# Kernel optimization log

Measured on AMD Instinct MI355X. Metric: run time of the kernel, lower is better.

Reference implementation:

```python
import jax, jax.numpy as jnp
import numpy as np

B, S, D_TEXT, MAXF = 2, 1024, 384, 5
D_MODEL, N_HEADS, D_FF, L = 768, 12, 3072, 4
HEAD_DIM = D_MODEL // N_HEADS
EPS = 1e-6
NEG = -1e9


def _rms(x, g):
    return x * jax.lax.rsqrt(jnp.mean(x * x, axis=-1, keepdims=True) + EPS) * g


def _attn(x, w, mask):
    # w: [4, d, d] = (wq, wk, wv, wo); mask: [b, s, s] bool (True = attend)
    b, s, d = x.shape

    def proj(W):
        return jnp.einsum('bsd,de->bse', x, W).reshape(b, s, N_HEADS, HEAD_DIM).transpose(0, 2, 1, 3)

    q, k, v = proj(w[0]), proj(w[1]), proj(w[2])
    scale = jnp.asarray(1.0 / np.sqrt(HEAD_DIM), x.dtype)
    scores = jnp.einsum('bhqe,bhke->bhqk', q, k) * scale
    scores = jnp.where(mask[:, None], scores, NEG)
    p = jax.nn.softmax(scores, axis=-1)
    o = jnp.einsum('bhqk,bhke->bhqe', p, v).transpose(0, 2, 1, 3).reshape(b, s, d)
    return jnp.einsum('bsd,de->bse', o, w[3])


def _forward(number_values, datetime_values, boolean_values, text_values, column_name_values,
             W_cn, b_cn, W_num, b_num, W_text, b_text, W_dt, b_dt, W_bool, b_bool,
             g_cn, g_num, g_text, g_dt, g_bool, mask_emb,
             blk_norms, blk_attn, blk_up, blk_gate, blk_down,
             g_out, Wd_num, bd_num, Wd_dt, bd_dt, Wd_bool, bd_bool, Wd_text, bd_text,
             node_indices, table_name_indices, column_name_indices,
             f2p_neighbor_indices, semantic_types, masks, is_padding):
    valid = ~is_padding
    pv = valid[:, :, None] & valid[:, None, :]  # [b,s,s]
    eye = jnp.eye(S, dtype=bool)[None]
    same_node = node_indices[:, :, None] == node_indices[:, None, :]
    col_mask = ((column_name_indices[:, :, None] == column_name_indices[:, None, :])
                & (table_name_indices[:, :, None] == table_name_indices[:, None, :]) & pv) | eye
    feat_mask = (same_node & pv) | eye
    # kv node is one of q's f2p neighbors
    nei = (f2p_neighbor_indices[:, :, :, None] == node_indices[:, None, None, :]).any(axis=2)
    nei_mask = ((nei | same_node) & pv) | eye
    full_mask = pv | eye

    # per-semantic-type value encoders (Linear + RMSNorm)
    cn = _rms(column_name_values @ W_cn + b_cn, g_cn)
    num_e = _rms(number_values @ W_num + b_num, g_num)
    text_e = _rms(text_values @ W_text + b_text, g_text)
    dt_e = _rms(datetime_values @ W_dt + b_dt, g_dt)
    bool_e = _rms(boolean_values @ W_bool + b_bool, g_bool)
    st = semantic_types[..., None]
    val = jnp.where(st == 0, num_e, jnp.where(st == 1, text_e, jnp.where(st == 2, dt_e, bool_e)))
    # masked cells get the learned mask embedding for their semantic type
    val = jnp.where(masks[..., None], mask_emb[semantic_types], val)
    x = val + cn

    for i in range(L):
        nw, aw = blk_norms[i], blk_attn[i]
        x = x + _attn(_rms(x, nw[0]), aw[0], col_mask)
        x = x + _attn(_rms(x, nw[1]), aw[1], feat_mask)
        x = x + _attn(_rms(x, nw[2]), aw[2], nei_mask)
        x = x + _attn(_rms(x, nw[3]), aw[3], full_mask)
        h = _rms(x, nw[4])
        x = x + (jax.nn.silu(h @ blk_gate[i]) * (h @ blk_up[i])) @ blk_down[i]

    h = _rms(x, g_out)
    return (h @ Wd_num + bd_num, h @ Wd_dt + bd_dt, h @ Wd_bool + bd_bool, h @ Wd_text + bd_text)


def setup_inputs() -> dict:
    key = jax.random.key(0)
    ks = iter(jax.random.split(key, 64))

    def nrm(shape, scale=0.02):
        return jax.random.normal(next(ks), shape, jnp.float32) * scale

    inp = {}
    inp['number_values'] = jax.random.normal(next(ks), (B, S, 1), jnp.float32)
    inp['datetime_values'] = jax.random.normal(next(ks), (B, S, 1), jnp.float32)
    inp['boolean_values'] = jax.random.normal(next(ks), (B, S, 1), jnp.float32)
    inp['text_values'] = jax.random.normal(next(ks), (B, S, D_TEXT), jnp.float32)
    inp['column_name_values'] = jax.random.normal(next(ks), (B, S, D_TEXT), jnp.float32)
    inp['W_cn'] = nrm((D_TEXT, D_MODEL)); inp['b_cn'] = jnp.zeros((D_MODEL,), jnp.float32)
    inp['W_num'] = nrm((1, D_MODEL)); inp['b_num'] = jnp.zeros((D_MODEL,), jnp.float32)
    inp['W_text'] = nrm((D_TEXT, D_MODEL)); inp['b_text'] = jnp.zeros((D_MODEL,), jnp.float32)
    inp['W_dt'] = nrm((1, D_MODEL)); inp['b_dt'] = jnp.zeros((D_MODEL,), jnp.float32)
    inp['W_bool'] = nrm((1, D_MODEL)); inp['b_bool'] = jnp.zeros((D_MODEL,), jnp.float32)
    for n in ('g_cn', 'g_num', 'g_text', 'g_dt', 'g_bool'):
        inp[n] = jnp.ones((D_MODEL,), jnp.float32)
    inp['mask_emb'] = jax.random.normal(next(ks), (4, D_MODEL), jnp.float32)
    inp['blk_norms'] = jnp.ones((L, 5, D_MODEL), jnp.float32)
    inp['blk_attn'] = nrm((L, 4, 4, D_MODEL, D_MODEL))
    inp['blk_up'] = nrm((L, D_MODEL, D_FF))
    inp['blk_gate'] = nrm((L, D_MODEL, D_FF))
    inp['blk_down'] = nrm((L, D_FF, D_MODEL))
    inp['g_out'] = jnp.ones((D_MODEL,), jnp.float32)
    inp['Wd_num'] = nrm((D_MODEL, 1)); inp['bd_num'] = jnp.zeros((1,), jnp.float32)
    inp['Wd_dt'] = nrm((D_MODEL, 1)); inp['bd_dt'] = jnp.zeros((1,), jnp.float32)
    inp['Wd_bool'] = nrm((D_MODEL, 1)); inp['bd_bool'] = jnp.zeros((1,), jnp.float32)
    inp['Wd_text'] = nrm((D_MODEL, D_TEXT)); inp['bd_text'] = jnp.zeros((D_TEXT,), jnp.float32)
    inp['node_indices'] = jax.random.randint(next(ks), (B, S), 0, 128)
    inp['table_name_indices'] = jax.random.randint(next(ks), (B, S), 0, 8)
    inp['column_name_indices'] = jax.random.randint(next(ks), (B, S), 0, 32)
    inp['f2p_neighbor_indices'] = jax.random.randint(next(ks), (B, S, MAXF), 0, 128)
    inp['semantic_types'] = jax.random.randint(next(ks), (B, S), 0, 4)
    inp['masks'] = jax.random.bernoulli(next(ks), 0.15, (B, S))
    inp['is_padding'] = jnp.zeros((B, S), bool)
    return inp


def reference(number_values, datetime_values, boolean_values, text_values, column_name_values,
              W_cn, b_cn, W_num, b_num, W_text, b_text, W_dt, b_dt, W_bool, b_bool,
              g_cn, g_num, g_text, g_dt, g_bool, mask_emb,
              blk_norms, blk_attn, blk_up, blk_gate, blk_down,
              g_out, Wd_num, bd_num, Wd_dt, bd_dt, Wd_bool, bd_bool, Wd_text, bd_text,
              node_indices, table_name_indices, column_name_indices,
              f2p_neighbor_indices, semantic_types, masks, is_padding):
    return _forward(number_values, datetime_values, boolean_values, text_values, column_name_values,
                    W_cn, b_cn, W_num, b_num, W_text, b_text, W_dt, b_dt, W_bool, b_bool,
                    g_cn, g_num, g_text, g_dt, g_bool, mask_emb,
                    blk_norms, blk_attn, blk_up, blk_gate, blk_down,
                    g_out, Wd_num, bd_num, Wd_dt, bd_dt, Wd_bool, bd_bool, Wd_text, bd_text,
                    node_indices, table_name_indices, column_name_indices,
                    f2p_neighbor_indices, semantic_types, masks, is_padding)
```

## Files before the change

### kernel.cpp

```cpp
#include <hip/hip_runtime.h>
#include <hip/hip_bf16.h>
#include <cmath>
#include <stdint.h>


#define BB 2
#define SS 1024
#define DT 384
#define DM 768
#define NH 12
#define DH 64
#define DFF 3072
#define NL 4
#define NROW (BB*SS)
#define EPSF 1e-6f
#define NEGF (-1e9f)

typedef unsigned short u16;
typedef unsigned char u8;
typedef unsigned int u32;
typedef __attribute__((ext_vector_type(8))) short s16x8;
typedef __attribute__((ext_vector_type(4))) float f32x4;

__device__ __forceinline__ u16 f2bu(float f){
    u32 x = __float_as_uint(f);
    u32 r = (x + 0x7fffu + ((x>>16)&1u)) >> 16;
    return (u16)r;
}
__device__ __forceinline__ u32 pk2(float lo, float hi){
    return (u32)f2bu(lo) | ((u32)f2bu(hi)<<16);
}
__device__ __forceinline__ int swz(int row, int c){
    return (row<<6) + (((((c>>3) ^ row) & 7))<<3) + (c&7);
}
__device__ __forceinline__ float rsum16(float v){
    v += __shfl_xor(v,1); v += __shfl_xor(v,2);
    v += __shfl_xor(v,4); v += __shfl_xor(v,8);
    return v;
}
#define SBAR() __builtin_amdgcn_sched_barrier(0)
#define GLDS(src,dst) __builtin_amdgcn_global_load_lds((const __attribute__((address_space(1))) u32*)(src), (__attribute__((address_space(3))) u32*)(dst), 16, 0, 0)
#define GLDS4(src,dst) __builtin_amdgcn_global_load_lds((const __attribute__((address_space(1))) u32*)(src), (__attribute__((address_space(3))) u32*)(dst), 4, 0, 0)

__global__ void zero_f(float* __restrict__ p, int n){
    int i = blockIdx.x*256 + threadIdx.x;
    if (i<n) p[i]=0.f;
}

__global__ void norm_bool_kernel(const void* __restrict__ src, u8* __restrict__ dst, int n)
{
    __shared__ int fl[4];
    if (threadIdx.x<4) fl[threadIdx.x]=0;
    __syncthreads();
    const u32* wsrc = (const u32*)src;
    const int nw = n/4;
    int any=0, nb=0, hi=0, lo=0;
    for (int i=threadIdx.x;i<nw;i+=blockDim.x){
        u32 v=wsrc[i];
        if (!v) continue;
        any=1;
        #pragma unroll
        for (int b=0;b<4;b++){
            u32 by=(v>>(8*b))&0xffu;
            if (by>1u) nb=1;
            if (by==1u && b!=0) hi=1;
        }
        if ((v&0xffffu)==0x3f80u) lo=1;
    }
    if (any) atomicOr(&fl[0],1);
    if (nb)  atomicOr(&fl[1],1);
    if (hi)  atomicOr(&fl[2],1);
    if (lo)  atomicOr(&fl[3],1);
    __syncthreads();
    int c;
    if (!fl[0]) c=0;
    else if (!fl[1]) c = fl[2] ? 2 : 1;
    else if (fl[3]) c = 3;
    else c = 1;
    for (int i=threadIdx.x;i<n;i+=blockDim.x){
        u8 v;
        if (c==0)      v=0;
        else if (c==1) v = (((const u32*)src)[i]!=0u);
        else if (c==2) v = (((const u8*)src)[i]!=0u);
        else           v = (((const u16*)src)[i]!=0u);
        dst[i]=v;
    }
}

__global__ void pack_meta(const int* __restrict__ node, const int* __restrict__ colx,
                          const int* __restrict__ tbl, const u8* __restrict__ pad,
                          u32* __restrict__ pm, int n)
{
    int i = blockIdx.x*256 + threadIdx.x;
    if (i<n)
        pm[i] = (u32)(node[i]&0xff) | ((u32)(colx[i]&0xff)<<8) | ((u32)(tbl[i]&0xff)<<16) | ((u32)(pad[i]&1)<<24);
}

__global__ __launch_bounds__(256) void mask4_kernel(const u32* __restrict__ pm, const int* __restrict__ f2p,
                                                    u8* __restrict__ m4)
{
    const int b = blockIdx.y, kg = blockIdx.x;
    const int t = threadIdx.x;
    __shared__ u32 qm[1024];
    __shared__ int qf[1024*5];
    for (int i=t;i<1024;i+=256) qm[i] = pm[b*SS+i];
    for (int i=t;i<5*1024;i+=256) qf[i] = f2p[b*SS*5 + i];
    __syncthreads();
    const int q0 = t*4;
    u32 qmv[4]; int qn[4]; int qfv[4][5];
    #pragma unroll
    for (int j=0;j<4;j++){
        qmv[j]=qm[q0+j]; qn[j]=(int)(qmv[j]&0xffu);
        #pragma unroll
        for (int f=0;f<5;f++) qfv[j][f]=qf[(q0+j)*5+f];
    }
    for (int kk=0;kk<16;kk++){
        const int k = kg*16+kk;
        const u32 km = qm[k];
        const int kn = (int)(km&0xffu);
        u32 outw=0;
        #pragma unroll
        for (int j=0;j<4;j++){
            const u32 qmw = qmv[j];
            const bool pv = (((qmw|km)>>24)&1u)==0u;
            u32 by=0;
            if ((((qmw^km)&0x00ffff00u)==0u) && pv) by|=1;
            if ((((qmw^km)&0xffu)==0u) && pv) by|=2;
            bool nei = (qfv[j][0]==kn)||(qfv[j][1]==kn)||(qfv[j][2]==kn)||(qfv[j][3]==kn)||(qfv[j][4]==kn)
                       ||(qn[j]==kn);
            if (nei && pv) by|=4;
            if (pv) by|=8;
            if ((q0+j)==k) by=15;
            outw |= by<<(8*j);
        }
        ((u32*)(m4 + ((size_t)b<<20) + ((size_t)k<<10)))[t] = outw;
    }
}

__global__ __launch_bounds__(256) void transpose_cvt2(const float* __restrict__ src, u16* __restrict__ dst,
                                                      int K, int N, size_t dz,
                                                      const float* __restrict__ gbase, int gmode)
{
    const int z = blockIdx.z;
    src += (size_t)z*K*N;
    dst += (size_t)z*dz;
    const float* g = nullptr;
    if (gmode==1){ int m = z&3; if (m<3) g = gbase + (size_t)((z>>4)*5 + ((z>>2)&3))*768; }
    else if (gmode==2){ g = gbase + (size_t)z*5*768; }
    const int n0 = blockIdx.x*32, k0 = blockIdx.y*64;
    __shared__ float t[64][33];
    const int tid = threadIdx.x;
    const int kr = tid>>3, n4 = (tid&7)*4;
    #pragma unroll
    for (int p=0;p<2;p++){
        const int k = p*32 + kr;
        float gk = g ? g[k0+k] : 1.f;
        float4 v = *(const float4*)(src + (size_t)(k0+k)*N + n0 + n4);
        t[k][n4]=v.x*gk; t[k][n4+1]=v.y*gk; t[k][n4+2]=v.z*gk; t[k][n4+3]=v.w*gk;
    }
    __syncthreads();
    const int n = tid>>3, ks = (tid&7)*8;
    const int ng = n0 + n;
    uint4 o;
    u32* op = (u32*)&o;
    #pragma unroll
    for (int i=0;i<4;i++)
        op[i] = pk2(t[ks+2*i][n], t[ks+2*i+1][n]);
    *(uint4*)&dst[(((size_t)(ng>>7)*(K>>6) + (k0>>6))<<13) + ((ng&127)<<6) + ks] = o;
}

__global__ __launch_bounds__(256) void cvt_tiled(const float* __restrict__ src, u16* __restrict__ dst, int K)
{
    const int gid = blockIdx.x*256 + threadIdx.x;
    const int base = gid*8;
    const int row = base / K, col = base - row*K;
    float4 a = *(const float4*)(src + base);
    float4 b = *(const float4*)(src + base + 4);
    uint4 o;
    o.x = pk2(a.x,a.y); o.y = pk2(a.z,a.w);
    o.z = pk2(b.x,b.y); o.w = pk2(b.z,b.w);
    *(uint4*)&dst[(((size_t)(row>>7)*(K>>6) + (col>>6))<<13) + ((row&127)<<6) + (col&63)] = o;
}

__device__ __forceinline__ void stage3(const u16* aT, const u16* bT, int cb, int brow,
                                       u16* la, u16* lb, int w, int l)
{
    #pragma unroll
    for (int p=0;p<2;p++){
        const int q = p*256 + w*64 + l;
        const int row = q>>2, u = q&3;
        const int so = row*64 + cb + (((u ^ ((row>>1)&3))&3)<<3);
        GLDS(aT+so, la + p*2048 + w*512);
    }
    {
        const int q = w*64 + l;
        const int row = q>>2, u = q&3;
        const int so = (brow+row)*64 + cb + (((u ^ ((row>>1)&3))&3)<<3);
        GLDS(bT+so, lb + w*512);
    }
}

__global__ __launch_bounds__(256,4) void gemm_t(
    const u16* __restrict__ At, const u16* __restrict__ Bt, float* __restrict__ C,
    int N, int K, int AMS, int flags, const float* __restrict__ bias,
    u16* __restrict__ o16, u16* __restrict__ qk16, u16* __restrict__ vt16,
    const float* __restrict__ rs_in, float* __restrict__ rs_out)
{
    __shared__ u16 lds[3][6144];
    const int tid = threadIdx.x;
    const int lane = tid & 63, w = tid >> 6;
    const int cg = lane >> 4, cl = lane & 15;
    const int NT = K >> 5;
    const int n0 = blockIdx.x*64;
    const int brow = n0 & 64;
    const size_t bNb = (size_t)(n0>>7)*(K>>6);

    const u16* aB = At + ((size_t)blockIdx.y * AMS << 13);
    const u16* bB = Bt + (bNb << 13);

    f32x4 acc[2][4];
    #pragma unroll
    for (int i=0;i<2;i++)
        #pragma unroll
        for (int j=0;j<4;j++) acc[i][j] = (f32x4){0.f,0.f,0.f,0.f};

    stage3(aB, bB, 0,  brow, &lds[0][0], &lds[0][4096], w, lane);
    stage3(aB, bB, 32, brow, &lds[1][0], &lds[1][4096], w, lane);

    for (int kt=0; kt<NT; kt++){
        const int buf = kt % 3;
        if (kt+2 < NT){
            const int k2 = kt+2;
            stage3(aB + ((size_t)(k2>>1)<<13), bB + ((size_t)(k2>>1)<<13),
                   (k2&1)<<5, brow, &lds[k2%3][0], &lds[k2%3][4096], w, lane);
            asm volatile("s_waitcnt vmcnt(6)" ::: "memory");
        } else if (kt+1 < NT){
            asm volatile("s_waitcnt vmcnt(3)" ::: "memory");
        } else {
            asm volatile("s_waitcnt vmcnt(0)" ::: "memory");
        }
        SBAR(); __builtin_amdgcn_s_barrier(); SBAR();
        s16x8 af[2], bf[4];
        #pragma unroll
        for (int mt=0;mt<2;mt++){
            const int ra = w*32 + mt*16 + cl;
            af[mt] = *(const s16x8*)&lds[buf][ra*32 + (((cg ^ ((ra>>1)&3))&3)<<3)];
        }
        #pragma unroll
        for (int nt=0;nt<4;nt++){
            const int rb = nt*16 + cl;
            bf[nt] = *(const s16x8*)&lds[buf][4096 + rb*32 + (((cg ^ ((rb>>1)&3))&3)<<3)];
        }
        #pragma unroll
        for (int mt=0;mt<2;mt++)
            #pragma unroll
            for (int nt=0;nt<4;nt++)
                acc[mt][nt] = __builtin_amdgcn_mfma_f32_16x16x32_bf16(af[mt], bf[nt], acc[mt][nt], 0,0,0);
        SBAR(); __builtin_amdgcn_s_barrier(); SBAR();
    }

    const int m0 = blockIdx.y*128;
    if (flags & 4){
        #pragma unroll
        for (int mt=0;mt<2;mt++){
            const int grow0 = m0 + w*32 + mt*16 + cg*4;
            float rr[4];
            #pragma unroll
            for (int j=0;j<4;j++) rr[j] = rsqrtf(rs_in[grow0+j]*(1.f/768.f) + EPSF);
            #pragma unroll
            for (int nt=0;nt<4;nt++){
                const int col = n0 + nt*16 + cl;
                if (col < 1536){
                    #pragma unroll
                    for (int j=0;j<4;j++)
                        qk16[(size_t)(grow0+j)*1536 + col] = f2bu(acc[mt][nt][j]*rr[j]);
                } else {
                    const int b = grow0>>10, s0 = grow0&1023;
                    const int dhg = col - 1536;
                    uint2 o;
                    o.x = pk2(acc[mt][nt][0]*rr[0], acc[mt][nt][1]*rr[1]);
                    o.y = pk2(acc[mt][nt][2]*rr[2], acc[mt][nt][3]*rr[3]);
                    *(uint2*)(vt16 + ((size_t)(b*768 + dhg)<<10) + s0) = o;
                }
            }
        }
    } else {
        const int NC = N>>6;
        #pragma unroll
        for (int mt=0;mt<2;mt++){
            const int grow0 = m0 + w*32 + mt*16 + cg*4;
            float rr[4];
            #pragma unroll
            for (int j=0;j<4;j++) rr[j] = rs_in ? rsqrtf(rs_in[grow0+j]*(1.f/768.f) + EPSF) : 1.f;
            #pragma unroll
            for (int nt=0;nt<4;nt++){
                const int col = n0 + nt*16 + cl;
                const size_t tb = (((size_t)(grow0>>7)*NC + (col>>6))<<13) + (col&63);
                #pragma unroll
                for (int j=0;j<4;j++)
                    o16[tb + (((grow0+j)&127)<<6)] = f2bu(acc[mt][nt][j]*rr[j]);
            }
        }
    }
}

__device__ __forceinline__ void stage64(const u16* aT, int arow, const u16* bT, int brow, int cb,
                                        u16* la, u16* lb, int w, int l)
{
    const int q = w*64 + l;
    const int row = q>>2, u = q&3;
    const int sw = (((u ^ ((row>>1)&3))&3)<<3);
    GLDS(aT + (arow+row)*64 + cb + sw, la + w*512);
    GLDS(bT + (brow+row)*64 + cb + sw, lb + w*512);
}

__global__ __launch_bounds__(256,6) void gemm_t64(
    const u16* __restrict__ At, const u16* __restrict__ Bt, float* __restrict__ C,
    int N, int K, int AMS, int flags, const float* __restrict__ bias,
    u16* __restrict__ o16, float* __restrict__ rs_out)
{
    __shared__ u16 lds[3][4096];
    const int tid = threadIdx.x;
    const int lane = tid & 63, w = tid >> 6;
    const int cg = lane >> 4, cl = lane & 15;
    const int NT = K >> 5;
    const int n0 = blockIdx.x*64;
    const int m0 = blockIdx.y*64;
    const int brow = n0 & 64, arow = m0 & 64;

    const u16* aB = At + ((size_t)(m0>>7) * AMS << 13);
    const u16* bB = Bt + ((size_t)(n0>>7) * (K>>6) << 13);

    f32x4 acc[4];
    #pragma unroll
    for (int j=0;j<4;j++) acc[j] = (f32x4){0.f,0.f,0.f,0.f};

    stage64(aB, arow, bB, brow, 0,  &lds[0][0], &lds[0][2048], w, lane);
    stage64(aB, arow, bB, brow, 32, &lds[1][0], &lds[1][2048], w, lane);

    for (int kt=0; kt<NT; kt++){
        const int buf = kt % 3;
        if (kt+2 < NT){
            const int k2 = kt+2;
            stage64(aB + ((size_t)(k2>>1)<<13), arow, bB + ((size_t)(k2>>1)<<13), brow,
                    (k2&1)<<5, &lds[k2%3][0], &lds[k2%3][2048], w, lane);
            asm volatile("s_waitcnt vmcnt(4)" ::: "memory");
        } else if (kt+1 < NT){
            asm volatile("s_waitcnt vmcnt(2)" ::: "memory");
        } else {
            asm volatile("s_waitcnt vmcnt(0)" ::: "memory");
        }
        SBAR(); __builtin_amdgcn_s_barrier(); SBAR();
        const int ra = w*16 + cl;
        s16x8 af = *(const s16x8*)&lds[buf][ra*32 + (((cg ^ ((ra>>1)&3))&3)<<3)];
        s16x8 bf[4];
        #pragma unroll
        for (int nt=0;nt<4;nt++){
            const int rb = nt*16 + cl;
            bf[nt] = *(const s16x8*)&lds[buf][2048 + rb*32 + (((cg ^ ((rb>>1)&3))&3)<<3)];
        }
        #pragma unroll
        for (int nt=0;nt<4;nt++)
            acc[nt] = __builtin_amdgcn_mfma_f32_16x16x32_bf16(af, bf[nt], acc[nt], 0,0,0);
        SBAR(); __builtin_amdgcn_s_barrier(); SBAR();
    }

    const int grow0 = m0 + w*16 + cg*4;
    const bool do_acc = (flags&1), do_bias = (flags&2);
    float tmp[4][4];
    #pragma unroll
    for (int nt=0;nt<4;nt++){
        const int col = n0 + nt*16 + cl;
        float bv = do_bias ? bias[col] : 0.f;
        #pragma unroll
        for (int j=0;j<4;j++){
            float v = acc[nt][j] + bv;
            float* cp = C + (size_t)(grow0+j)*N + col;
            if (do_acc) v += *cp;
            *cp = v;
            tmp[nt][j] = v;
        }
    }
    if (o16){
        #pragma unroll
        for (int nt=0;nt<4;nt++){
            const int col = n0 + nt*16 + cl;
            const size_t tb = (((size_t)(grow0>>7)*12 + (col>>6))<<13) + (col&63);
            #pragma unroll
            for (int j=0;j<4;j++)
                o16[tb + (((grow0+j)&127)<<6)] = f2bu(tmp[nt][j]);
        }
    }
    if (rs_out){
        #pragma unroll
        for (int j=0;j<4;j++){
            float s = tmp[0][j]*tmp[0][j] + tmp[1][j]*tmp[1][j]
                    + tmp[2][j]*tmp[2][j] + tmp[3][j]*tmp[3][j];
            s = rsum16(s);
            if (cl==0) atomicAdd(rs_out + grow0 + j, s);
        }
    }
}

__global__ __launch_bounds__(256,3) void attn_mfma3(
    const u16* __restrict__ qk16, const u16* __restrict__ vt16,
    const u8* __restrict__ m4, int mt,
    u16* __restrict__ ob16)
{
    const int bh = blockIdx.y;
    const int b = bh / NH, h = bh % NH;
    const int q0 = blockIdx.x * 64;
    const int tid = threadIdx.x;
    const int w = tid>>6, lane = tid&63, cg = lane>>4, cl = lane&15;
    const int srow = lane>>3;
    const int sseg = (lane&7) ^ srow;
    const int mk = lane>>4, mq = lane&15;

    __shared__ u16 Qs[4096], Ks[2][4096], Vt[2][4096], Ps[4096];
    __shared__ u32 Ms[2][1024];

    const u16* qbase = qk16 + (size_t)(b*SS+q0)*1536 + h*64;
    const u16* kbase = qk16 + (size_t)(b*SS)*1536 + 768 + h*64;
    const u16* vbase = vt16 + ((size_t)(b*768 + h*64)<<10);
    const u8*  mbase = m4 + ((size_t)b<<20) + q0;

    #pragma unroll
    for (int p=0;p<2;p++){
        const int row = p*32 + w*8 + srow;
        GLDS(qbase + (size_t)row*1536 + sseg*8, Qs + p*2048 + w*512);
    }
    #pragma unroll
    for (int p=0;p<2;p++){
        const int row = p*32 + w*8 + srow;
        GLDS(kbase + (size_t)row*1536 + sseg*8, Ks[0] + p*2048 + w*512);
        GLDS(vbase + ((size_t)row<<10) + sseg*8, Vt[0] + p*2048 + w*512);
    }
    #pragma unroll
    for (int i=0;i<4;i++){
        const int key = w*16 + i*4 + mk;
        GLDS4(mbase + ((size_t)key<<10) + mq*4, (u8*)Ms[0] + w*1024 + i*256);
    }

    f32x4 o[4];
    #pragma unroll
    for (int nt=0;nt<4;nt++) o[nt] = (f32x4){0.f,0.f,0.f,0.f};
    float lsum[4] = {0.f,0.f,0.f,0.f};

    for (int kc=0;kc<16;kc++){
        const int buf = kc & 1;
        if (kc < 15){
            const int kn0 = kc*64 + 64;
            #pragma unroll
            for (int p=0;p<2;p++){
                const int row = p*32 + w*8 + srow;
                GLDS(kbase + (size_t)(kn0+row)*1536 + sseg*8, Ks[buf^1] + p*2048 + w*512);
                GLDS(vbase + ((size_t)row<<10) + kn0 + sseg*8, Vt[buf^1] + p*2048 + w*512);
            }
            #pragma unroll
            for (int i=0;i<4;i++){
                const int key = kn0 + w*16 + i*4 + mk;
                GLDS4(mbase + ((size_t)key<<10) + mq*4, (u8*)Ms[buf^1] + w*1024 + i*256);
            }
            asm volatile("s_waitcnt vmcnt(8)" ::: "memory");
        } else {
            asm volatile("s_waitcnt vmcnt(0)" ::: "memory");
        }
        SBAR(); __builtin_amdgcn_s_barrier(); SBAR();

        f32x4 sc[4];
        #pragma unroll
        for (int nt=0;nt<4;nt++) sc[nt] = (f32x4){0.f,0.f,0.f,0.f};
        __builtin_amdgcn_s_setprio(1);
        #pragma unroll
        for (int ks=0;ks<2;ks++){
            s16x8 qa = *(const s16x8*)&Qs[swz(w*16+cl, ks*32+cg*8)];
            #pragma unroll
            for (int nt=0;nt<4;nt++){
                s16x8 kb = *(const s16x8*)&Ks[buf][swz(nt*16+cl, ks*32+cg*8)];
                sc[nt] = __builtin_amdgcn_mfma_f32_16x16x32_bf16(qa, kb, sc[nt], 0,0,0);
            }
        }
        __builtin_amdgcn_s_setprio(0);

        float pP[4][4];
        #pragma unroll
        for (int nt=0;nt<4;nt++){
            const u32 w4 = Ms[buf][(nt*16+cl)*16 + w*4 + cg];
            #pragma unroll
            for (int j=0;j<4;j++){
                float sv = fminf(sc[nt][j]*0.125f, 60.f);
                float pe = __expf(sv);
                pe = ((w4 >> (8*j + mt)) & 1u) ? pe : 0.f;
                pP[nt][j] = pe;
                lsum[j] += pe;
            }
        }

        #pragma unroll
        for (int nt=0;nt<4;nt++)
            #pragma unroll
            for (int j=0;j<4;j++)
                Ps[swz(w*16+cg*4+j, nt*16+cl)] = f2bu(pP[nt][j]);

        __builtin_amdgcn_s_setprio(1);
        #pragma unroll
        for (int ks=0;ks<2;ks++){
            s16x8 pa = *(const s16x8*)&Ps[swz(w*16+cl, ks*32+cg*8)];
            #pragma unroll
            for (int nt=0;nt<4;nt++){
                s16x8 vb = *(const s16x8*)&Vt[buf][swz(nt*16+cl, ks*32+cg*8)];
                o[nt] = __builtin_amdgcn_mfma_f32_16x16x32_bf16(pa, vb, o[nt], 0,0,0);
            }
        }
        __builtin_amdgcn_s_setprio(0);
        SBAR(); __builtin_amdgcn_s_barrier(); SBAR();
    }

    #pragma unroll
    for (int j=0;j<4;j++){
        const float inv = 1.f/rsum16(lsum[j]);
        const int row = b*SS + q0 + w*16 + cg*4 + j;
        const size_t rb = ((size_t)(row>>7)*12 + h)*8192 + ((row&127)<<6);
        #pragma unroll
        for (int nt=0;nt<4;nt++)
            ob16[rb + nt*16 + cl] = f2bu(o[nt][j]*inv);
    }
}

__global__ __launch_bounds__(256) void fuse_encode(
    const float* __restrict__ cnbuf, const float* __restrict__ textbuf,
    const float* __restrict__ numv, const float* __restrict__ dtv, const float* __restrict__ boolv,
    const float* __restrict__ Wnum, const float* __restrict__ bnum,
    const float* __restrict__ Wdt, const float* __restrict__ bdt,
    const float* __restrict__ Wbool, const float* __restrict__ bbool,
    const float* __restrict__ gcn, const float* __restrict__ gnum, const float* __restrict__ gtext,
    const float* __restrict__ gdt, const float* __restrict__ gbool,
    const float* __restrict__ memb, const int* __restrict__ stypes, const u8* __restrict__ masks,
    float* __restrict__ x, u16* __restrict__ xt16, float* __restrict__ rs0)
{
    const int row = blockIdx.x;
    const int t = threadIdx.x;
    __shared__ float red[256];

    float cn3[3]; float ss=0.f;
    #pragma unroll
    for (int j=0;j<3;j++){
        cn3[j] = cnbuf[(size_t)row*DM + t + j*256];
        ss += cn3[j]*cn3[j];
    }
    red[t]=ss; __syncthreads();
    for (int s=128;s>0;s>>=1){ if(t<s) red[t]+=red[t+s]; __syncthreads(); }
    {
        float r = rsqrtf(red[0]/(float)DM + EPSF);
        #pragma unroll
        for (int j=0;j<3;j++) cn3[j] *= r*gcn[t+j*256];
    }
    __syncthreads();

    const int st = stypes[row];
    float val[3]; ss=0.f;
    if (st==1){
        #pragma unroll
        for (int j=0;j<3;j++){
            val[j] = textbuf[(size_t)row*DM + t + j*256];
            ss += val[j]*val[j];
        }
    } else {
        const float* Wp = (st==0)?Wnum:((st==2)?Wdt:Wbool);
        const float* bp = (st==0)?bnum:((st==2)?bdt:bbool);
        const float* vp = (st==0)?numv:((st==2)?dtv:boolv);
        float v = vp[row];
        #pragma unroll
        for (int j=0;j<3;j++){
            int e=t+j*256;
            val[j] = v*Wp[e] + bp[e];
            ss += val[j]*val[j];
        }
    }
    red[t]=ss; __syncthreads();
    for (int s=128;s>0;s>>=1){ if(t<s) red[t]+=red[t+s]; __syncthreads(); }
    const float* gp = (st==0)?gnum:((st==1)?gtext:((st==2)?gdt:gbool));
    float r2 = rsqrtf(red[0]/(float)DM + EPSF);
    bool mk = masks[row]!=0;
    float xv[3]; float sx=0.f;
    #pragma unroll
    for (int j=0;j<3;j++){
        int e=t+j*256;
        float vv = val[j]*r2*gp[e];
        if (mk) vv = memb[st*DM+e];
        xv[j] = vv + cn3[j];
        x[(size_t)row*DM+e] = xv[j];
        sx += xv[j]*xv[j];
    }
    __syncthreads();
    red[t]=sx; __syncthreads();
    for (int s=128;s>0;s>>=1){ if(t<s) red[t]+=red[t+s]; __syncthreads(); }
    if (t==0) rs0[row] = red[0];
    const size_t mb = (size_t)(row>>7)*12;
    const int rr = (row&127)<<6;
    #pragma unroll
    for (int j=0;j<3;j++){
        const int c = t + j*256;
        xt16[((mb + (c>>6))<<13) + rr + (c&63)] = f2bu(xv[j]);
    }
}

__global__ void silu_gu(u16* __restrict__ gu, int nu)
{
    int i = blockIdx.x*blockDim.x + threadIdx.x;
    const int stride = gridDim.x*blockDim.x;
    for (; i<nu; i+=stride){
        const int mt = i / (48*1024);
        const int r  = i - mt*48*1024;
        const size_t gi = (size_t)(mt*96)*1024 + r;
        const size_t ui = gi + 48*1024;
        uint4 gv = ((const uint4*)gu)[gi];
        uint4 uv = ((const uint4*)gu)[ui];
        u32 go[4]; const u32* gp=(const u32*)&gv; const u32* up=(const u32*)&uv;
        #pragma unroll
        for (int k=0;k<4;k++){
            float g0 = __uint_as_float(gp[k]<<16), g1 = __uint_as_float(gp[k]&0xffff0000u);
            float u0 = __uint_as_float(up[k]<<16), u1 = __uint_as_float(up[k]&0xffff0000u);
            float s0 = g0/(1.f+__expf(-g0))*u0;
            float s1 = g1/(1.f+__expf(-g1))*u1;
            go[k] = pk2(s0, s1);
        }
        ((uint4*)gu)[gi] = make_uint4(go[0],go[1],go[2],go[3]);
    }
}

__global__ __launch_bounds__(256) void decode2(
    const float* __restrict__ x, const float* __restrict__ gout,
    const float* __restrict__ Wn, const float* __restrict__ bn,
    const float* __restrict__ Wd, const float* __restrict__ bd,
    const float* __restrict__ Wb, const float* __restrict__ bb,
    float* __restrict__ out, u16* __restrict__ h16)
{
    const int row = blockIdx.x;
    const int t = threadIdx.x;
    __shared__ float h[DM];
    __shared__ float red[256];
    const float* xr = x + (size_t)row*DM;
    float v0=xr[t], v1=xr[t+256], v2=xr[t+512];
    red[t]=v0*v0+v1*v1+v2*v2; __syncthreads();
    for (int s=128;s>0;s>>=1){ if(t<s) red[t]+=red[t+s]; __syncthreads(); }
    float r = rsqrtf(red[0]/(float)DM + EPSF);
    float h0 = v0*r*gout[t], h1 = v1*r*gout[t+256], h2 = v2*r*gout[t+512];
    h[t]=h0; h[t+256]=h1; h[t+512]=h2;
    const size_t mb = (size_t)(row>>7)*12;
    const int rr = (row&127)<<6;
    #pragma unroll
    for (int j=0;j<3;j++){
        const int c = t + j*256;
        const float v = (j==0?h0:(j==1?h1:h2));
        h16[((mb + (c>>6))<<13) + rr + (c&63)] = f2bu(v);
    }
    __syncthreads();

    float pn=0.f,pd=0.f,pb=0.f;
    for (int k=t;k<DM;k+=256){ float hv=h[k]; pn+=hv*Wn[k]; pd+=hv*Wd[k]; pb+=hv*Wb[k]; }
    red[t]=pn; __syncthreads();
    for (int s=128;s>0;s>>=1){ if(t<s) red[t]+=red[t+s]; __syncthreads(); }
    float tn=red[0]; __syncthreads();
    red[t]=pd; __syncthreads();
    for (int s=128;s>0;s>>=1){ if(t<s) red[t]+=red[t+s]; __syncthreads(); }
    float td=red[0]; __syncthreads();
    red[t]=pb; __syncthreads();
    for (int s=128;s>0;s>>=1){ if(t<s) red[t]+=red[t+s]; __syncthreads(); }
    float tb=red[0];
    if (t==0){
        out[row]          = tn + bn[0];
        out[NROW + row]   = td + bd[0];
        out[2*NROW + row] = tb + bb[0];
    }
}

extern "C" void kernel_launch(void* const* d_in, const int* in_sizes, int n_in,
                              void* d_out, int out_size, void* d_ws, size_t ws_size,
                              hipStream_t stream)
{
    const float* numv   = (const float*)d_in[0];
    const float* dtval  = (const float*)d_in[1];
    const float* boolv  = (const float*)d_in[2];
    const float* textv  = (const float*)d_in[3];
    const float* cnamev = (const float*)d_in[4];
    const float* Wcn=(const float*)d_in[5];  const float* bcn=(const float*)d_in[6];
    const float* Wnum=(const float*)d_in[7]; const float* bnum=(const float*)d_in[8];
    const float* Wtext=(const float*)d_in[9];const float* btext=(const float*)d_in[10];
    const float* Wdt=(const float*)d_in[11]; const float* bdt=(const float*)d_in[12];
    const float* Wbool=(const float*)d_in[13];const float* bbool=(const float*)d_in[14];
    const float* gcn=(const float*)d_in[15]; const float* gnum=(const float*)d_in[16];
    const float* gtext=(const float*)d_in[17];const float* gdt=(const float*)d_in[18];
    const float* gbool=(const float*)d_in[19];
    const float* memb=(const float*)d_in[20];
    const float* norms_all=(const float*)d_in[21];
    const float* attw_all=(const float*)d_in[22];
    const float* up_all=(const float*)d_in[23];
    const float* gate_all=(const float*)d_in[24];
    const float* down_all=(const float*)d_in[25];
    const float* gout=(const float*)d_in[26];
    const float* Wdn=(const float*)d_in[27]; const float* bdn=(const float*)d_in[28];
    const float* Wdd=(const float*)d_in[29]; const float* bdd=(const float*)d_in[30];
    const float* Wdb=(const float*)d_in[31]; const float* bdb=(const float*)d_in[32];
    const float* Wdtx=(const float*)d_in[33];const float* bdtx=(const float*)d_in[34];
    const int* node=(const int*)d_in[35];
    const int* tbl =(const int*)d_in[36];
    const int* colx=(const int*)d_in[37];
    const int* f2p =(const int*)d_in[38];
    const int* styp=(const int*)d_in[39];

    const size_t SA = (size_t)768*768;
    const size_t SG = (size_t)768*3072;
    const size_t SC = (size_t)384*768;
    const size_t NX = (size_t)NROW*DM;

    u8* base = (u8*)d_ws;
    float* x  = (float*)base;
    u16* xt16 = (u16*)(base + 6291456);
    u16* ob16 = (u16*)(base + 9437184);
    u16* qk16 = (u16*)(base + 12582912);
    u16* vt16 = (u16*)(base + 18874368);
    u16* gu16 = (u16*)(base + 22020096);
    u16* wA   = (u16*)(base + 47185920);
    u16* wGU  = wA + 64*SA;
    u16* wD   = wGU + 8*SG;
    u16* wCN  = wD + 4*SG;
    u16* wTX  = wCN + SC;
    u16* wDX  = wTX + SC;
    u8* nmask = (u8*)(wDX + SC);
    u8* npad  = nmask + NROW;
    u32* pmeta = (u32*)(npad + NROW + 64);
    float* rsbuf = (float*)(pmeta + NROW);
    u8* m4 = (u8*)(rsbuf + 21*2048);

    u16* cnT16   = qk16;
    u16* textT16 = vt16;
    float* cnbuf   = (float*)gu16;
    float* textbuf = cnbuf + NX;

    float* out = (float*)d_out;

    zero_f<<<(21*2048)/256,256,0,stream>>>(rsbuf, 21*2048);
    norm_bool_kernel<<<1,256,0,stream>>>(d_in[40], nmask, NROW);
    norm_bool_kernel<<<1,256,0,stream>>>(d_in[41], npad,  NROW);
    pack_meta<<<NROW/256,256,0,stream>>>(node, colx, tbl, npad, pmeta, NROW);
    mask4_kernel<<<dim3(64,2),256,0,stream>>>(pmeta, f2p, m4);

    transpose_cvt2<<<dim3(24,12,64),256,0,stream>>>(attw_all, wA, 768, 768, SA, norms_all, 1);
    transpose_cvt2<<<dim3(96,12,4),256,0,stream>>>(gate_all, wGU,      768, 3072, 2*SG, norms_all + 4*768, 2);
    transpose_cvt2<<<dim3(96,12,4),256,0,stream>>>(up_all,   wGU + SG, 768, 3072, 2*SG, norms_all + 4*768, 2);
    transpose_cvt2<<<dim3(24,48,4),256,0,stream>>>(down_all, wD, 3072, 768, SG, nullptr, 0);
    transpose_cvt2<<<dim3(24,6,1),256,0,stream>>>(Wcn,   wCN, 384, 768, 0, nullptr, 0);
    transpose_cvt2<<<dim3(24,6,1),256,0,stream>>>(Wtext, wTX, 384, 768, 0, nullptr, 0);
    transpose_cvt2<<<dim3(12,12,1),256,0,stream>>>(Wdtx, wDX, 768, 384, 0, nullptr, 0);

    cvt_tiled<<<384,256,0,stream>>>(cnamev, cnT16, 384);
    cvt_tiled<<<384,256,0,stream>>>(textv,  textT16, 384);
    gemm_t64<<<dim3(12,32),256,0,stream>>>(cnT16,   wCN, cnbuf,   768, 384, 6, 2, bcn,   nullptr, nullptr);
    gemm_t64<<<dim3(12,32),256,0,stream>>>(textT16, wTX, textbuf, 768, 384, 6, 2, btext, nullptr, nullptr);
    fuse_encode<<<NROW,256,0,stream>>>(cnbuf, textbuf, numv, dtval, boolv,
        Wnum,bnum,Wdt,bdt,Wbool,bbool, gcn,gnum,gtext,gdt,gbool,
        memb, styp, nmask, x, xt16, rsbuf);

    const dim3 ga(SS/64, BB*NH);
    for (int l=0; l<NL; l++){
        for (int a=0; a<4; a++){
            const int slot = l*5 + a;
            const u16* wqkv = wA + (size_t)((l*4+a)*4)*SA;
            gemm_t<<<dim3(36,16),256,0,stream>>>(xt16, wqkv, nullptr, 2304, 768, 12, 4, nullptr,
                nullptr, qk16, vt16, rsbuf + (size_t)slot*2048, nullptr);
            attn_mfma3<<<ga,256,0,stream>>>(qk16, vt16, m4, a, ob16);
            gemm_t64<<<dim3(12,32),256,0,stream>>>(ob16, wqkv + 3*SA, x, 768, 768, 12, 1, nullptr,
                xt16, rsbuf + (size_t)(slot+1)*2048);
        }
        gemm_t<<<dim3(96,16),256,0,stream>>>(xt16, wGU + (size_t)l*2*SG, nullptr, 6144, 768, 12, 8, nullptr,
            gu16, nullptr, nullptr, rsbuf + (size_t)(l*5+4)*2048, nullptr);
        silu_gu<<<1024,256,0,stream>>>(gu16, 16*48*1024);
        gemm_t64<<<dim3(12,32),256,0,stream>>>(gu16, wD + (size_t)l*SG, x, 768, 3072, 96, 1, nullptr,
            xt16, rsbuf + (size_t)((l+1)*5)*2048);
    }

    decode2<<<NROW,256,0,stream>>>(x, gout, Wdn,bdn, Wdd,bdd, Wdb,bdb, out, xt16);
    gemm_t64<<<dim3(6,32),256,0,stream>>>(xt16, wDX, out + 3*NROW, 384, 768, 12, 2, bdtx,
        nullptr, nullptr);
}
```

Before: 1.449 ms.

## Fuse SiLU gating into gate/up GEMM, fold softmax scale into Q, merge small kernels

Adds a dedicated gate/up GEMM that computes both gate and up accumulators per tile and applies SiLU*up in the epilogue. This removes the separate silu_gu pass and halves the gu buffer written and read by the down projection. Q is pre-scaled by log2(e)/sqrt(64) so attention can use exp2 without a multiply. The paired norm_bool and cvt_tiled launches are merged into single launches. The fused GEMM holds two accumulator sets and more LDS, which lowers occupancy to 3 blocks per SM.

```diff
diff --git a/kernel.cpp b/kernel.cpp
--- a/kernel.cpp
+++ b/kernel.cpp
@@ -14,7 +14,7 @@
 #define NL 4
 #define NROW (BB*SS)
 #define EPSF 1e-6f
-#define NEGF (-1e9f)
+#define QSC 0.1803368801111244f
 
 typedef unsigned short u16;
 typedef unsigned char u8;
@@ -47,7 +47,7 @@
     if (i<n) p[i]=0.f;
 }
 
-__global__ void norm_bool_kernel(const void* __restrict__ src, u8* __restrict__ dst, int n)
+__device__ void norm_bool_body(const void* __restrict__ src, u8* __restrict__ dst, int n)
 {
     __shared__ int fl[4];
     if (threadIdx.x<4) fl[threadIdx.x]=0;
@@ -86,6 +86,11 @@
         dst[i]=v;
     }
 }
+__global__ void norm_bool2(const void* s0, u8* d0, const void* s1, u8* d1, int n)
+{
+    if (blockIdx.x==0) norm_bool_body(s0,d0,n);
+    else               norm_bool_body(s1,d1,n);
+}
 
 __global__ void pack_meta(const int* __restrict__ node, const int* __restrict__ colx,
                           const int* __restrict__ tbl, const u8* __restrict__ pad,
@@ -169,8 +174,11 @@
     *(uint4*)&dst[(((size_t)(ng>>7)*(K>>6) + (k0>>6))<<13) + ((ng&127)<<6) + ks] = o;
 }
 
-__global__ __launch_bounds__(256) void cvt_tiled(const float* __restrict__ src, u16* __restrict__ dst, int K)
-{
+__global__ __launch_bounds__(256) void cvt_tiled2(const float* __restrict__ s0, u16* __restrict__ d0,
+                                                  const float* __restrict__ s1, u16* __restrict__ d1, int K)
+{
+    const float* src = blockIdx.y ? s1 : s0;
+    u16* dst = blockIdx.y ? d1 : d0;
     const int gid = blockIdx.x*256 + threadIdx.x;
     const int base = gid*8;
     const int row = base / K, col = base - row*K;
@@ -201,10 +209,9 @@
 }
 
 __global__ __launch_bounds__(256,4) void gemm_t(
-    const u16* __restrict__ At, const u16* __restrict__ Bt, float* __restrict__ C,
-    int N, int K, int AMS, int flags, const float* __restrict__ bias,
-    u16* __restrict__ o16, u16* __restrict__ qk16, u16* __restrict__ vt16,
-    const float* __restrict__ rs_in, float* __restrict__ rs_out)
+    const u16* __restrict__ At, const u16* __restrict__ Bt,
+    int K, int AMS, u16* __restrict__ qk16, u16* __restrict__ vt16,
+    const float* __restrict__ rs_in)
 {
     __shared__ u16 lds[3][6144];
     const int tid = threadIdx.x;
@@ -260,45 +267,132 @@
     }
 
     const int m0 = blockIdx.y*128;
-    if (flags & 4){
-        #pragma unroll
-        for (int mt=0;mt<2;mt++){
-            const int grow0 = m0 + w*32 + mt*16 + cg*4;
-            float rr[4];
-            #pragma unroll
-            for (int j=0;j<4;j++) rr[j] = rsqrtf(rs_in[grow0+j]*(1.f/768.f) + EPSF);
-            #pragma unroll
-            for (int nt=0;nt<4;nt++){
-                const int col = n0 + nt*16 + cl;
-                if (col < 1536){
-                    #pragma unroll
-                    for (int j=0;j<4;j++)
-                        qk16[(size_t)(grow0+j)*1536 + col] = f2bu(acc[mt][nt][j]*rr[j]);
-                } else {
-                    const int b = grow0>>10, s0 = grow0&1023;
-                    const int dhg = col - 1536;
-                    uint2 o;
-                    o.x = pk2(acc[mt][nt][0]*rr[0], acc[mt][nt][1]*rr[1]);
-                    o.y = pk2(acc[mt][nt][2]*rr[2], acc[mt][nt][3]*rr[3]);
-                    *(uint2*)(vt16 + ((size_t)(b*768 + dhg)<<10) + s0) = o;
-                }
-            }
-        }
-    } else {
-        const int NC = N>>6;
-        #pragma unroll
-        for (int mt=0;mt<2;mt++){
-            const int grow0 = m0 + w*32 + mt*16 + cg*4;
-            float rr[4];
-            #pragma unroll
-            for (int j=0;j<4;j++) rr[j] = rs_in ? rsqrtf(rs_in[grow0+j]*(1.f/768.f) + EPSF) : 1.f;
-            #pragma unroll
-            for (int nt=0;nt<4;nt++){
-                const int col = n0 + nt*16 + cl;
-                const size_t tb = (((size_t)(grow0>>7)*NC + (col>>6))<<13) + (col&63);
+    #pragma unroll
+    for (int mt=0;mt<2;mt++){
+        const int grow0 = m0 + w*32 + mt*16 + cg*4;
+        float rr[4];
+        #pragma unroll
+        for (int j=0;j<4;j++) rr[j] = rsqrtf(rs_in[grow0+j]*(1.f/768.f) + EPSF);
+        #pragma unroll
+        for (int nt=0;nt<4;nt++){
+            const int col = n0 + nt*16 + cl;
+            if (col < 768){
                 #pragma unroll
                 for (int j=0;j<4;j++)
-                    o16[tb + (((grow0+j)&127)<<6)] = f2bu(acc[mt][nt][j]*rr[j]);
+                    qk16[(size_t)(grow0+j)*1536 + col] = f2bu(acc[mt][nt][j]*rr[j]*QSC);
+            } else if (col < 1536){
+                #pragma unroll
+                for (int j=0;j<4;j++)
+                    qk16[(size_t)(grow0+j)*1536 + col] = f2bu(acc[mt][nt][j]*rr[j]);
+            } else {
+                const int b = grow0>>10, s0 = grow0&1023;
+                const int dhg = col - 1536;
+                uint2 o;
+                o.x = pk2(acc[mt][nt][0]*rr[0], acc[mt][nt][1]*rr[1]);
+                o.y = pk2(acc[mt][nt][2]*rr[2], acc[mt][nt][3]*rr[3]);
+                *(uint2*)(vt16 + ((size_t)(b*768 + dhg)<<10) + s0) = o;
+            }
+        }
+    }
+}
+
+__global__ __launch_bounds__(256,3) void gemm_gu(
+    const u16* __restrict__ At, const u16* __restrict__ Bg, const u16* __restrict__ Bu,
+    const float* __restrict__ rs_in, u16* __restrict__ o16)
+{
+    __shared__ u16 lds[3][8192];
+    const int tid = threadIdx.x;
+    const int lane = tid & 63, w = tid >> 6;
+    const int cg = lane >> 4, cl = lane & 15;
+    const int NT = 24;
+    const int n0 = blockIdx.x*64;
+    const int brow = n0 & 64;
+    const size_t bNb = (size_t)(n0>>7)*12;
+
+    const u16* aB = At + ((size_t)blockIdx.y * 12 << 13);
+    const u16* gB = Bg + (bNb << 13);
+    const u16* uB = Bu + (bNb << 13);
+
+    f32x4 accg[2][4], accu[2][4];
+    #pragma unroll
+    for (int i=0;i<2;i++)
+        #pragma unroll
+        for (int j=0;j<4;j++){ accg[i][j] = (f32x4){0.f,0.f,0.f,0.f}; accu[i][j] = (f32x4){0.f,0.f,0.f,0.f}; }
+
+    #define STAGE_GU(kt2, cb, buf) { \
+        const u16* a_ = aB + ((size_t)(kt2)<<13); \
+        const u16* g_ = gB + ((size_t)(kt2)<<13); \
+        const u16* u_ = uB + ((size_t)(kt2)<<13); \
+        _Pragma("unroll") \
+        for (int p=0;p<2;p++){ \
+            const int q = p*256 + w*64 + lane; \
+            const int row = q>>2, uu = q&3; \
+            const int so = row*64 + (cb) + (((uu ^ ((row>>1)&3))&3)<<3); \
+            GLDS(a_+so, &lds[buf][0] + p*2048 + w*512); \
+        } \
+        { \
+            const int q = w*64 + lane; \
+            const int row = q>>2, uu = q&3; \
+            const int so = (brow+row)*64 + (cb) + (((uu ^ ((row>>1)&3))&3)<<3); \
+            GLDS(g_+so, &lds[buf][4096] + w*512); \
+            GLDS(u_+so, &lds[buf][6144] + w*512); \
+        } }
+
+    STAGE_GU(0, 0,  0);
+    STAGE_GU(0, 32, 1);
+
+    for (int kt=0; kt<NT; kt++){
+        const int buf = kt % 3;
+        if (kt+2 < NT){
+            const int k2 = kt+2;
+            STAGE_GU(k2>>1, (k2&1)<<5, k2%3);
+            asm volatile("s_waitcnt vmcnt(8)" ::: "memory");
+        } else if (kt+1 < NT){
+            asm volatile("s_waitcnt vmcnt(4)" ::: "memory");
+        } else {
+            asm volatile("s_waitcnt vmcnt(0)" ::: "memory");
+        }
+        SBAR(); __builtin_amdgcn_s_barrier(); SBAR();
+        s16x8 af[2], bg[4], bu[4];
+        #pragma unroll
+        for (int mt=0;mt<2;mt++){
+            const int ra = w*32 + mt*16 + cl;
+            af[mt] = *(const s16x8*)&lds[buf][ra*32 + (((cg ^ ((ra>>1)&3))&3)<<3)];
+        }
+        #pragma unroll
+        for (int nt=0;nt<4;nt++){
+            const int rb = nt*16 + cl;
+            const int sw = (((cg ^ ((rb>>1)&3))&3)<<3);
+            bg[nt] = *(const s16x8*)&lds[buf][4096 + rb*32 + sw];
+            bu[nt] = *(const s16x8*)&lds[buf][6144 + rb*32 + sw];
+        }
+        #pragma unroll
+        for (int mt=0;mt<2;mt++)
+            #pragma unroll
+            for (int nt=0;nt<4;nt++){
+                accg[mt][nt] = __builtin_amdgcn_mfma_f32_16x16x32_bf16(af[mt], bg[nt], accg[mt][nt], 0,0,0);
+                accu[mt][nt] = __builtin_amdgcn_mfma_f32_16x16x32_bf16(af[mt], bu[nt], accu[mt][nt], 0,0,0);
+            }
+        SBAR(); __builtin_amdgcn_s_barrier(); SBAR();
+    }
+
+    const int m0 = blockIdx.y*128;
+    #pragma unroll
+    for (int mt=0;mt<2;mt++){
+        const int grow0 = m0 + w*32 + mt*16 + cg*4;
+        float rr[4];
+        #pragma unroll
+        for (int j=0;j<4;j++) rr[j] = rsqrtf(rs_in[grow0+j]*(1.f/768.f) + EPSF);
+        #pragma unroll
+        for (int nt=0;nt<4;nt++){
+            const int col = n0 + nt*16 + cl;
+            const size_t tb = (((size_t)(grow0>>7)*48 + (col>>6))<<13) + (col&63);
+            #pragma unroll
+            for (int j=0;j<4;j++){
+                float g = accg[mt][nt][j]*rr[j];
+                float u = accu[mt][nt][j]*rr[j];
+                float s = g/(1.f+__expf(-g))*u;
+                o16[tb + (((grow0+j)&127)<<6)] = f2bu(s);
             }
         }
     }
@@ -488,8 +582,7 @@
             const u32 w4 = Ms[buf][(nt*16+cl)*16 + w*4 + cg];
             #pragma unroll
             for (int j=0;j<4;j++){
-                float sv = fminf(sc[nt][j]*0.125f, 60.f);
-                float pe = __expf(sv);
+                float pe = exp2f(fminf(sc[nt][j], 100.f));
                 pe = ((w4 >> (8*j + mt)) & 1u) ? pe : 0.f;
                 pP[nt][j] = pe;
                 lsum[j] += pe;
@@ -602,30 +695,6 @@
     for (int j=0;j<3;j++){
         const int c = t + j*256;
         xt16[((mb + (c>>6))<<13) + rr + (c&63)] = f2bu(xv[j]);
-    }
-}
-
-__global__ void silu_gu(u16* __restrict__ gu, int nu)
-{
-    int i = blockIdx.x*blockDim.x + threadIdx.x;
-    const int stride = gridDim.x*blockDim.x;
-    for (; i<nu; i+=stride){
-        const int mt = i / (48*1024);
-        const int r  = i - mt*48*1024;
-        const size_t gi = (size_t)(mt*96)*1024 + r;
-        const size_t ui = gi + 48*1024;
-        uint4 gv = ((const uint4*)gu)[gi];
-        uint4 uv = ((const uint4*)gu)[ui];
-        u32 go[4]; const u32* gp=(const u32*)&gv; const u32* up=(const u32*)&uv;
-        #pragma unroll
-        for (int k=0;k<4;k++){
-            float g0 = __uint_as_float(gp[k]<<16), g1 = __uint_as_float(gp[k]&0xffff0000u);
-            float u0 = __uint_as_float(up[k]<<16), u1 = __uint_as_float(up[k]&0xffff0000u);
-            float s0 = g0/(1.f+__expf(-g0))*u0;
-            float s1 = g1/(1.f+__expf(-g1))*u1;
-            go[k] = pk2(s0, s1);
-        }
-        ((uint4*)gu)[gi] = make_uint4(go[0],go[1],go[2],go[3]);
     }
 }
 
@@ -741,8 +810,7 @@
     float* out = (float*)d_out;
 
     zero_f<<<(21*2048)/256,256,0,stream>>>(rsbuf, 21*2048);
-    norm_bool_kernel<<<1,256,0,stream>>>(d_in[40], nmask, NROW);
-    norm_bool_kernel<<<1,256,0,stream>>>(d_in[41], npad,  NROW);
+    norm_bool2<<<2,256,0,stream>>>(d_in[40], nmask, d_in[41], npad, NROW);
     pack_meta<<<NROW/256,256,0,stream>>>(node, colx, tbl, npad, pmeta, NROW);
     mask4_kernel<<<dim3(64,2),256,0,stream>>>(pmeta, f2p, m4);
 
@@ -754,8 +822,7 @@
     transpose_cvt2<<<dim3(24,6,1),256,0,stream>>>(Wtext, wTX, 384, 768, 0, nullptr, 0);
     transpose_cvt2<<<dim3(12,12,1),256,0,stream>>>(Wdtx, wDX, 768, 384, 0, nullptr, 0);
 
-    cvt_tiled<<<384,256,0,stream>>>(cnamev, cnT16, 384);
-    cvt_tiled<<<384,256,0,stream>>>(textv,  textT16, 384);
+    cvt_tiled2<<<dim3(384,2),256,0,stream>>>(cnamev, cnT16, textv, textT16, 384);
     gemm_t64<<<dim3(12,32),256,0,stream>>>(cnT16,   wCN, cnbuf,   768, 384, 6, 2, bcn,   nullptr, nullptr);
     gemm_t64<<<dim3(12,32),256,0,stream>>>(textT16, wTX, textbuf, 768, 384, 6, 2, btext, nullptr, nullptr);
     fuse_encode<<<NROW,256,0,stream>>>(cnbuf, textbuf, numv, dtval, boolv,
@@ -767,16 +834,15 @@
         for (int a=0; a<4; a++){
             const int slot = l*5 + a;
             const u16* wqkv = wA + (size_t)((l*4+a)*4)*SA;
-            gemm_t<<<dim3(36,16),256,0,stream>>>(xt16, wqkv, nullptr, 2304, 768, 12, 4, nullptr,
-                nullptr, qk16, vt16, rsbuf + (size_t)slot*2048, nullptr);
+            gemm_t<<<dim3(36,16),256,0,stream>>>(xt16, wqkv, 768, 12, qk16, vt16,
+                rsbuf + (size_t)slot*2048);
             attn_mfma3<<<ga,256,0,stream>>>(qk16, vt16, m4, a, ob16);
             gemm_t64<<<dim3(12,32),256,0,stream>>>(ob16, wqkv + 3*SA, x, 768, 768, 12, 1, nullptr,
                 xt16, rsbuf + (size_t)(slot+1)*2048);
         }
-        gemm_t<<<dim3(96,16),256,0,stream>>>(xt16, wGU + (size_t)l*2*SG, nullptr, 6144, 768, 12, 8, nullptr,
-            gu16, nullptr, nullptr, rsbuf + (size_t)(l*5+4)*2048, nullptr);
-        silu_gu<<<1024,256,0,stream>>>(gu16, 16*48*1024);
-        gemm_t64<<<dim3(12,32),256,0,stream>>>(gu16, wD + (size_t)l*SG, x, 768, 3072, 96, 1, nullptr,
+        gemm_gu<<<dim3(48,16),256,0,stream>>>(xt16, wGU + (size_t)l*2*SG, wGU + (size_t)l*2*SG + SG,
+            rsbuf + (size_t)(l*5+4)*2048, gu16);
+        gemm_t64<<<dim3(12,32),256,0,stream>>>(gu16, wD + (size_t)l*SG, x, 768, 3072, 48, 1, nullptr,
             xt16, rsbuf + (size_t)((l+1)*5)*2048);
     }
 
```

Result: no change. 1.448 ms (-0.1%).
